# Performance work log

Measured on AMD Instinct MI355X. Metric: run time of the kernel, lower is better.

The kernel has to match this reference:

```python
import jax, jax.numpy as jnp
import numpy as np

FP8_E4M3_MAX = 448.0
BLOCK_SIZE = 128


def _block_quant_dequant_e4m3(x, block_size=BLOCK_SIZE):
    """Per-block (along last dim) FP8 E4M3 fake quantize: returns dequantized fp32."""
    M, K = x.shape
    nb = K // block_size
    xb = x.reshape(M, nb, block_size)
    amax = jnp.clip(jnp.max(jnp.abs(xb), axis=-1, keepdims=True), 1e-12, None)
    scale = FP8_E4M3_MAX / amax  # per-block scale, [M, nb, 1]
    q = jnp.clip(xb * scale, -FP8_E4M3_MAX, FP8_E4M3_MAX).astype(jnp.float8_e4m3fn)
    deq = q.astype(jnp.float32) / scale
    return deq.reshape(M, K)


def _dual_quantize_weight(w, block_size=BLOCK_SIZE):
    """TCFP-12 dual quantization: FP8 hi component + FP8-quantized residual (lo)."""
    w_hi = _block_quant_dequant_e4m3(w, block_size)
    residual = w - w_hi
    w_lo = _block_quant_dequant_e4m3(residual, block_size)
    return w_hi + w_lo


def setup_inputs() -> dict:
    key = jax.random.key(0)
    k1, k2, k3 = jax.random.split(key, 3)
    B, T, DIN, DOUT = 8, 4096, 1024, 1024
    x = jax.random.normal(k1, (B, T, DIN), dtype=jnp.float32)
    weight = jax.random.normal(k2, (DOUT, DIN), dtype=jnp.float32) * 0.02
    bias = jax.random.normal(k3, (DOUT,), dtype=jnp.float32) * 0.01
    return {"x": x, "weight": weight, "bias": bias}


def reference(x, weight, bias):
    # Block-quantize activations (fake-quant, per 128-col block, E4M3)
    B, T, DIN = x.shape
    x2d = x.reshape(-1, DIN)
    x_q = _block_quant_dequant_e4m3(x2d, BLOCK_SIZE)
    # Dual-quantize weight: hi + residual lo components
    w_q = _dual_quantize_weight(weight, BLOCK_SIZE)
    # Block-scaled GEMM (dequantized reference math) + bias
    out2d = x_q @ w_q.T + bias
    return out2d.reshape(B, T, -1)
```

## Files before the change

### kernel.cpp

```cpp
#include <hip/hip_runtime.h>
#include <hip/hip_bf16.h>

typedef __bf16 bf16x8 __attribute__((ext_vector_type(8)));
typedef float  f32x4  __attribute__((ext_vector_type(4)));

#define GLOAD_LDS16(gptr, lptr)                                                  \
  __builtin_amdgcn_global_load_lds(                                              \
      (const __attribute__((address_space(1))) void*)(gptr),                     \
      (__attribute__((address_space(3))) void*)(lptr), 16, 0, 0)

__device__ __forceinline__ unsigned short f2bf(float f) {
  __hip_bfloat16 h = __float2bfloat16(f);
  return __builtin_bit_cast(unsigned short, h);
}

__device__ __forceinline__ float groupmax32(float v) {
  v = fmaxf(v, __shfl_xor(v, 1));
  v = fmaxf(v, __shfl_xor(v, 2));
  v = fmaxf(v, __shfl_xor(v, 4));
  v = fmaxf(v, __shfl_xor(v, 8));
  v = fmaxf(v, __shfl_xor(v, 16));
  return v;
}

__device__ __forceinline__ void fq_e4m3_4(const float* __restrict__ in,
                                          float* __restrict__ out) {
  float am = fmaxf(fmaxf(fabsf(in[0]), fabsf(in[1])),
                   fmaxf(fabsf(in[2]), fabsf(in[3])));
  am = groupmax32(am);
  am = fmaxf(am, 1e-12f);
  const float scale = 448.0f / am;
  const float inv   = am * (1.0f / 448.0f);
  float c0 = fminf(fmaxf(in[0] * scale, -448.0f), 448.0f);
  float c1 = fminf(fmaxf(in[1] * scale, -448.0f), 448.0f);
  float c2 = fminf(fmaxf(in[2] * scale, -448.0f), 448.0f);
  float c3 = fminf(fmaxf(in[3] * scale, -448.0f), 448.0f);
  int pk = __builtin_amdgcn_cvt_pk_fp8_f32(c0, c1, 0, false);
  pk = __builtin_amdgcn_cvt_pk_fp8_f32(c2, c3, pk, true);
  out[0] = __builtin_amdgcn_cvt_f32_fp8(pk, 0) * inv;
  out[1] = __builtin_amdgcn_cvt_f32_fp8(pk, 1) * inv;
  out[2] = __builtin_amdgcn_cvt_f32_fp8(pk, 2) * inv;
  out[3] = __builtin_amdgcn_cvt_f32_fp8(pk, 3) * inv;
}

#define XROWS 16
__global__ __launch_bounds__(256) void quant_x_k(const float* __restrict__ x,
                                                 unsigned short* __restrict__ xq) {
  const int tid = threadIdx.x;
  const size_t row0 = (size_t)blockIdx.x * XROWS;
#pragma unroll 4
  for (int j = 0; j < XROWS; ++j) {
    const size_t row = row0 + j;
    const float4 v = ((const float4*)(x + row * 1024))[tid];
    float in[4] = {v.x, v.y, v.z, v.w};
    float dq[4];
    fq_e4m3_4(in, dq);
    union { ushort4 u; unsigned short s[4]; } pk;
    pk.s[0] = f2bf(dq[0]); pk.s[1] = f2bf(dq[1]);
    pk.s[2] = f2bf(dq[2]); pk.s[3] = f2bf(dq[3]);
    ((ushort4*)(xq + row * 1024))[tid] = pk.u;
  }
}

#define WROWS 4
__global__ __launch_bounds__(256) void quant_w_k(const float* __restrict__ w,
                                                 unsigned short* __restrict__ wq) {
  const int tid = threadIdx.x;
  const size_t row0 = (size_t)blockIdx.x * WROWS;
#pragma unroll
  for (int j = 0; j < WROWS; ++j) {
    const size_t row = row0 + j;
    const float4 v = ((const float4*)(w + row * 1024))[tid];
    float in[4] = {v.x, v.y, v.z, v.w};
    float hi[4], res[4], lo[4];
    fq_e4m3_4(in, hi);
#pragma unroll
    for (int i = 0; i < 4; ++i) res[i] = in[i] - hi[i];
    fq_e4m3_4(res, lo);
    union { ushort4 u; unsigned short s[4]; } pk;
#pragma unroll
    for (int i = 0; i < 4; ++i) pk.s[i] = f2bf(hi[i] + lo[i]);
    ((ushort4*)(wq + row * 1024))[tid] = pk.u;
  }
}

#define BM 128
#define BN 128
#define BK 64

__global__ __launch_bounds__(256) void gemm_bt_bias(
    const unsigned short* __restrict__ A,
    const unsigned short* __restrict__ B,
    const float* __restrict__ bias,
    float* __restrict__ C,
    int M, int N, int K) {
  __shared__ unsigned short ldsA[BM * BK];
  __shared__ unsigned short ldsB[BN * BK];

  const int tid  = threadIdx.x;
  const int wave = tid >> 6;
  const int lane = tid & 63;
  const int nbn  = N / BN;
  const int nbm  = M / BM;

  int bm, bn;
  if ((nbm & 7) == 0) {
    const int xcd = blockIdx.x & 7;
    const int j   = blockIdx.x >> 3;
    bn = j % nbn;
    bm = xcd * (nbm >> 3) + j / nbn;
  } else {
    bn = blockIdx.x % nbn;
    bm = blockIdx.x / nbn;
  }

  const int wr = wave >> 1;
  const int wc = wave & 1;

  f32x4 acc[4][4] = {};

  const int rload = wave * 32 + (lane >> 3);
  const int cload = (((lane & 7) ^ (lane >> 3)) * 8);
  const unsigned short* gA = A + (size_t)(bm * BM + rload) * K + cload;
  const unsigned short* gB = B + (size_t)(bn * BN + rload) * K + cload;
  unsigned short* lA = ldsA + wave * 2048 + lane * 8;
  unsigned short* lB = ldsB + wave * 2048 + lane * 8;

  for (int kt = 0; kt < K; kt += BK) {
    __syncthreads();
#pragma unroll
    for (int t = 0; t < 4; ++t) {
      GLOAD_LDS16(gA + (size_t)(t * 8) * K + kt, lA + t * 512);
      GLOAD_LDS16(gB + (size_t)(t * 8) * K + kt, lB + t * 512);
    }
    __syncthreads();

    const int fRow = lane & 15;
    const int sw   = fRow & 7;
#pragma unroll
    for (int kc = 0; kc < 2; ++kc) {
      const int c = kc * 4 + (lane >> 4);
      const int sOff = ((c ^ sw) * 8);
      bf16x8 af[4], bfr[4];
#pragma unroll
      for (int i = 0; i < 4; ++i)
        af[i] = *(const bf16x8*)&ldsA[(wr * 64 + i * 16 + fRow) * BK + sOff];
#pragma unroll
      for (int j = 0; j < 4; ++j)
        bfr[j] = *(const bf16x8*)&ldsB[(wc * 64 + j * 16 + fRow) * BK + sOff];
#pragma unroll
      for (int i = 0; i < 4; ++i)
#pragma unroll
        for (int j = 0; j < 4; ++j)
          acc[i][j] = __builtin_amdgcn_mfma_f32_16x16x32_bf16(af[i], bfr[j],
                                                              acc[i][j], 0, 0, 0);
    }
  }

  const int    n0 = bn * BN + wc * 64 + (lane & 15);
  const size_t m0 = (size_t)bm * BM + wr * 64 + ((lane >> 4) << 2);
#pragma unroll
  for (int j = 0; j < 4; ++j) {
    const int col = n0 + j * 16;
    const float bv = bias[col];
#pragma unroll
    for (int i = 0; i < 4; ++i) {
      const size_t base = (m0 + (size_t)i * 16) * N + col;
#pragma unroll
      for (int r = 0; r < 4; ++r)
        C[base + (size_t)r * N] = acc[i][j][r] + bv;
    }
  }
}

extern "C" void kernel_launch(void* const* d_in, const int* in_sizes, int n_in,
                              void* d_out, int out_size, void* d_ws, size_t ws_size,
                              hipStream_t stream) {
  const float* x    = (const float*)d_in[0];
  const float* w    = (const float*)d_in[1];
  const float* bias = (const float*)d_in[2];

  const int DOUT = in_sizes[2];
  const int DIN  = in_sizes[1] / DOUT;
  const int M    = in_sizes[0] / DIN;

  unsigned short* xq = (unsigned short*)d_ws;
  unsigned short* wq = xq + (size_t)M * DIN;

  hipLaunchKernelGGL(quant_x_k, dim3(M / XROWS), dim3(256), 0, stream, x, xq);
  hipLaunchKernelGGL(quant_w_k, dim3(DOUT / WROWS), dim3(256), 0, stream, w, wq);

  const int grid = (M / BM) * (DOUT / BN);
  hipLaunchKernelGGL(gemm_bt_bias, dim3(grid), dim3(256), 0, stream,
                     xq, wq, bias, (float*)d_out, M, DOUT, DIN);
}
```

Before: 328.6 us.

## Double-buffer GEMM LDS tiles and give each quant thread a full 32-element slice

The GEMM main loop now uses two LDS buffers. The global-to-LDS load of the next K tile is issued before the MFMA work on the current tile, so the kernel no longer stalls on each load. LDS use doubles and there is still one barrier per tile. The quantization kernels now have each thread handle 32 contiguous floats, so one 128-element block spans only 4 lanes. That cuts the cross-lane reduction to two shuffles, at the cost of more registers per thread and strided per-lane global accesses.

Measured after the change: 320.3 us. 1.03x faster.

```diff
diff --git a/kernel.cpp b/kernel.cpp
--- a/kernel.cpp
+++ b/kernel.cpp
@@ -14,73 +14,68 @@
   return __builtin_bit_cast(unsigned short, h);
 }
 
-__device__ __forceinline__ float groupmax32(float v) {
-  v = fmaxf(v, __shfl_xor(v, 1));
-  v = fmaxf(v, __shfl_xor(v, 2));
-  v = fmaxf(v, __shfl_xor(v, 4));
-  v = fmaxf(v, __shfl_xor(v, 8));
-  v = fmaxf(v, __shfl_xor(v, 16));
-  return v;
-}
-
-__device__ __forceinline__ void fq_e4m3_4(const float* __restrict__ in,
-                                          float* __restrict__ out) {
-  float am = fmaxf(fmaxf(fabsf(in[0]), fabsf(in[1])),
-                   fmaxf(fabsf(in[2]), fabsf(in[3])));
-  am = groupmax32(am);
+__device__ __forceinline__ void fq32(float* __restrict__ v) {
+  float am = 0.0f;
+#pragma unroll
+  for (int i = 0; i < 32; ++i) am = fmaxf(am, fabsf(v[i]));
+  am = fmaxf(am, __shfl_xor(am, 1));
+  am = fmaxf(am, __shfl_xor(am, 2));
   am = fmaxf(am, 1e-12f);
   const float scale = 448.0f / am;
   const float inv   = am * (1.0f / 448.0f);
-  float c0 = fminf(fmaxf(in[0] * scale, -448.0f), 448.0f);
-  float c1 = fminf(fmaxf(in[1] * scale, -448.0f), 448.0f);
-  float c2 = fminf(fmaxf(in[2] * scale, -448.0f), 448.0f);
-  float c3 = fminf(fmaxf(in[3] * scale, -448.0f), 448.0f);
-  int pk = __builtin_amdgcn_cvt_pk_fp8_f32(c0, c1, 0, false);
-  pk = __builtin_amdgcn_cvt_pk_fp8_f32(c2, c3, pk, true);
-  out[0] = __builtin_amdgcn_cvt_f32_fp8(pk, 0) * inv;
-  out[1] = __builtin_amdgcn_cvt_f32_fp8(pk, 1) * inv;
-  out[2] = __builtin_amdgcn_cvt_f32_fp8(pk, 2) * inv;
-  out[3] = __builtin_amdgcn_cvt_f32_fp8(pk, 3) * inv;
-}
-
-#define XROWS 16
+#pragma unroll
+  for (int i = 0; i < 32; i += 4) {
+    float c0 = fminf(fmaxf(v[i + 0] * scale, -448.0f), 448.0f);
+    float c1 = fminf(fmaxf(v[i + 1] * scale, -448.0f), 448.0f);
+    float c2 = fminf(fmaxf(v[i + 2] * scale, -448.0f), 448.0f);
+    float c3 = fminf(fmaxf(v[i + 3] * scale, -448.0f), 448.0f);
+    int pk = __builtin_amdgcn_cvt_pk_fp8_f32(c0, c1, 0, false);
+    pk = __builtin_amdgcn_cvt_pk_fp8_f32(c2, c3, pk, true);
+    v[i + 0] = __builtin_amdgcn_cvt_f32_fp8(pk, 0) * inv;
+    v[i + 1] = __builtin_amdgcn_cvt_f32_fp8(pk, 1) * inv;
+    v[i + 2] = __builtin_amdgcn_cvt_f32_fp8(pk, 2) * inv;
+    v[i + 3] = __builtin_amdgcn_cvt_f32_fp8(pk, 3) * inv;
+  }
+}
+
 __global__ __launch_bounds__(256) void quant_x_k(const float* __restrict__ x,
                                                  unsigned short* __restrict__ xq) {
-  const int tid = threadIdx.x;
-  const size_t row0 = (size_t)blockIdx.x * XROWS;
-#pragma unroll 4
-  for (int j = 0; j < XROWS; ++j) {
-    const size_t row = row0 + j;
-    const float4 v = ((const float4*)(x + row * 1024))[tid];
-    float in[4] = {v.x, v.y, v.z, v.w};
-    float dq[4];
-    fq_e4m3_4(in, dq);
-    union { ushort4 u; unsigned short s[4]; } pk;
-    pk.s[0] = f2bf(dq[0]); pk.s[1] = f2bf(dq[1]);
-    pk.s[2] = f2bf(dq[2]); pk.s[3] = f2bf(dq[3]);
-    ((ushort4*)(xq + row * 1024))[tid] = pk.u;
-  }
-}
-
-#define WROWS 4
+  const size_t u   = (size_t)blockIdx.x * 256 + threadIdx.x;
+  const size_t off = u * 32;
+  float v[32];
+#pragma unroll
+  for (int i = 0; i < 8; ++i)
+    *(float4*)&v[i * 4] = ((const float4*)(x + off))[i];
+  fq32(v);
+  union { uint4 q; unsigned short s[8]; } pk;
+#pragma unroll
+  for (int g = 0; g < 4; ++g) {
+#pragma unroll
+    for (int e = 0; e < 8; ++e) pk.s[e] = f2bf(v[g * 8 + e]);
+    ((uint4*)(xq + off))[g] = pk.q;
+  }
+}
+
 __global__ __launch_bounds__(256) void quant_w_k(const float* __restrict__ w,
                                                  unsigned short* __restrict__ wq) {
-  const int tid = threadIdx.x;
-  const size_t row0 = (size_t)blockIdx.x * WROWS;
-#pragma unroll
-  for (int j = 0; j < WROWS; ++j) {
-    const size_t row = row0 + j;
-    const float4 v = ((const float4*)(w + row * 1024))[tid];
-    float in[4] = {v.x, v.y, v.z, v.w};
-    float hi[4], res[4], lo[4];
-    fq_e4m3_4(in, hi);
-#pragma unroll
-    for (int i = 0; i < 4; ++i) res[i] = in[i] - hi[i];
-    fq_e4m3_4(res, lo);
-    union { ushort4 u; unsigned short s[4]; } pk;
-#pragma unroll
-    for (int i = 0; i < 4; ++i) pk.s[i] = f2bf(hi[i] + lo[i]);
-    ((ushort4*)(wq + row * 1024))[tid] = pk.u;
+  const size_t u   = (size_t)blockIdx.x * 256 + threadIdx.x;
+  const size_t off = u * 32;
+  float a[32], h[32], r[32];
+#pragma unroll
+  for (int i = 0; i < 8; ++i)
+    *(float4*)&a[i * 4] = ((const float4*)(w + off))[i];
+#pragma unroll
+  for (int i = 0; i < 32; ++i) h[i] = a[i];
+  fq32(h);
+#pragma unroll
+  for (int i = 0; i < 32; ++i) r[i] = a[i] - h[i];
+  fq32(r);
+  union { uint4 q; unsigned short s[8]; } pk;
+#pragma unroll
+  for (int g = 0; g < 4; ++g) {
+#pragma unroll
+    for (int e = 0; e < 8; ++e) pk.s[e] = f2bf(h[g * 8 + e] + r[g * 8 + e]);
+    ((uint4*)(wq + off))[g] = pk.q;
   }
 }
 
@@ -94,8 +89,8 @@
     const float* __restrict__ bias,
     float* __restrict__ C,
     int M, int N, int K) {
-  __shared__ unsigned short ldsA[BM * BK];
-  __shared__ unsigned short ldsB[BN * BK];
+  __shared__ unsigned short ldsA[2 * BM * BK];
+  __shared__ unsigned short ldsB[2 * BN * BK];
 
   const int tid  = threadIdx.x;
   const int wave = tid >> 6;
@@ -126,28 +121,32 @@
   unsigned short* lA = ldsA + wave * 2048 + lane * 8;
   unsigned short* lB = ldsB + wave * 2048 + lane * 8;
 
-  for (int kt = 0; kt < K; kt += BK) {
-    __syncthreads();
+  auto stage = [&](int it, int buf) {
+    const unsigned short* pA = gA + (size_t)it * BK;
+    const unsigned short* pB = gB + (size_t)it * BK;
+    unsigned short* dA = lA + buf * (BM * BK);
+    unsigned short* dB = lB + buf * (BN * BK);
 #pragma unroll
     for (int t = 0; t < 4; ++t) {
-      GLOAD_LDS16(gA + (size_t)(t * 8) * K + kt, lA + t * 512);
-      GLOAD_LDS16(gB + (size_t)(t * 8) * K + kt, lB + t * 512);
+      GLOAD_LDS16(pA + (size_t)(t * 8) * K, dA + t * 512);
+      GLOAD_LDS16(pB + (size_t)(t * 8) * K, dB + t * 512);
     }
-    __syncthreads();
-
+  };
+
+  auto compute = [&](const unsigned short* bA, const unsigned short* bB) {
     const int fRow = lane & 15;
     const int sw   = fRow & 7;
 #pragma unroll
     for (int kc = 0; kc < 2; ++kc) {
-      const int c = kc * 4 + (lane >> 4);
+      const int c    = kc * 4 + (lane >> 4);
       const int sOff = ((c ^ sw) * 8);
       bf16x8 af[4], bfr[4];
 #pragma unroll
       for (int i = 0; i < 4; ++i)
-        af[i] = *(const bf16x8*)&ldsA[(wr * 64 + i * 16 + fRow) * BK + sOff];
+        af[i] = *(const bf16x8*)&bA[(wr * 64 + i * 16 + fRow) * BK + sOff];
 #pragma unroll
       for (int j = 0; j < 4; ++j)
-        bfr[j] = *(const bf16x8*)&ldsB[(wc * 64 + j * 16 + fRow) * BK + sOff];
+        bfr[j] = *(const bf16x8*)&bB[(wc * 64 + j * 16 + fRow) * BK + sOff];
 #pragma unroll
       for (int i = 0; i < 4; ++i)
 #pragma unroll
@@ -155,6 +154,17 @@
           acc[i][j] = __builtin_amdgcn_mfma_f32_16x16x32_bf16(af[i], bfr[j],
                                                               acc[i][j], 0, 0, 0);
     }
+  };
+
+  stage(0, 0);
+  const int niter = K / BK;
+  for (int it = 0; it < niter; it += 2) {
+    __syncthreads();
+    if (it + 1 < niter) stage(it + 1, 1);
+    compute(ldsA, ldsB);
+    __syncthreads();
+    if (it + 2 < niter) stage(it + 2, 0);
+    compute(ldsA + BM * BK, ldsB + BN * BK);
   }
 
   const int    n0 = bn * BN + wc * 64 + (lane & 15);
@@ -187,8 +197,10 @@
   unsigned short* xq = (unsigned short*)d_ws;
   unsigned short* wq = xq + (size_t)M * DIN;
 
-  hipLaunchKernelGGL(quant_x_k, dim3(M / XROWS), dim3(256), 0, stream, x, xq);
-  hipLaunchKernelGGL(quant_w_k, dim3(DOUT / WROWS), dim3(256), 0, stream, w, wq);
+  hipLaunchKernelGGL(quant_x_k, dim3((size_t)M * DIN / 32 / 256), dim3(256), 0,
+                     stream, x, xq);
+  hipLaunchKernelGGL(quant_w_k, dim3((size_t)DOUT * DIN / 32 / 256), dim3(256), 0,
+                     stream, w, wq);
 
   const int grid = (M / BM) * (DOUT / BN);
   hipLaunchKernelGGL(gemm_bt_bias, dim3(grid), dim3(256), 0, stream,
```
